# Kernel optimization log

Hardware: AMD Instinct MI355X
Metric: run time of the kernel (lower is better)

The kernel has to match this reference:

```python
import jax, jax.numpy as jnp
import numpy as np

K = 3            # kernel_size
S = 4            # up_factor
VMAX = 1.0
TAU = 0.5
CENTER_BIAS = 2.5
SMOOTH_RES = 0.15
C_IN = 21
HIDDEN = 48
B_, H0, W0 = 4, 81, 81
CTR = K // 2      # = 1, also GL recursion depth M


def _dir_step_diff(k):
    """Precompute (base_pos - base_neg) per direction/step: [8, M+1, k, k]."""
    c = k // 2
    dirs = np.array([[1, 0], [1, 1], [0, 1], [-1, 1], [-1, 0], [-1, -1], [0, -1], [1, -1]], np.float32)
    dirs = dirs / (np.linalg.norm(dirs, axis=1, keepdims=True) + 1e-8)
    yy, xx = np.meshgrid(np.arange(k), np.arange(k), indexing='ij')
    rel = np.stack([yy - c, xx - c], -1).astype(np.float32)
    diff = np.zeros((8, c + 1, k, k), np.float32)
    for d in range(8):
        v = dirs[d]
        proj = rel[..., 0] * v[1] + rel[..., 1] * v[0]
        step = np.clip(np.round(proj), -c, c).astype(np.int64)
        for m in range(c + 1):
            diff[d, m] = (step == m).astype(np.float32) - (step == -m).astype(np.float32)
    return diff

DIFF = jnp.asarray(_dir_step_diff(K))  # [8, M+1, K, K]


def conv3x3(x, w, b):
    y = jax.lax.conv_general_dilated(x, w, (1, 1), 'SAME',
                                     dimension_numbers=('NCHW', 'OIHW', 'NCHW'))
    return y + b[None, :, None, None]


def bilinear_up(x, s):
    """F.interpolate(scale_factor=s, mode='bilinear', align_corners=True)."""
    B, C, h, w = x.shape
    H, W = h * s, w * s
    ys = jnp.linspace(0.0, h - 1.0, H)
    xs = jnp.linspace(0.0, w - 1.0, W)
    y0 = jnp.clip(jnp.floor(ys).astype(jnp.int32), 0, h - 2)
    x0 = jnp.clip(jnp.floor(xs).astype(jnp.int32), 0, w - 2)
    wy = (ys - y0)[:, None]
    wx = (xs - x0)[None, :]
    x00 = x[:, :, y0][:, :, :, x0]
    x01 = x[:, :, y0][:, :, :, x0 + 1]
    x10 = x[:, :, y0 + 1][:, :, :, x0]
    x11 = x[:, :, y0 + 1][:, :, :, x0 + 1]
    return (x00 * (1 - wy) * (1 - wx) + x01 * (1 - wy) * wx
            + x10 * wy * (1 - wx) + x11 * wy * wx)


def setup_inputs() -> dict:
    key = jax.random.key(0)
    ks = jax.random.split(key, 6)
    wn = lambda k, shape: jax.random.normal(k, shape, jnp.float32) * 0.05
    return {
        'x': jax.random.normal(ks[0], (B_, C_IN, H0, W0), jnp.float32),
        'w1o': wn(ks[1], (HIDDEN, C_IN, 3, 3)), 'b1o': jnp.zeros((HIDDEN,), jnp.float32),
        'w2o': wn(ks[2], (8, HIDDEN, 3, 3)), 'b2o': jnp.zeros((8,), jnp.float32),
        'w1g': wn(ks[3], (HIDDEN, C_IN, 3, 3)), 'b1g': jnp.zeros((HIDDEN,), jnp.float32),
        'w2g': wn(ks[4], (1, HIDDEN, 3, 3)), 'b2g': jnp.zeros((1,), jnp.float32),
        'beta': jnp.asarray(1.6, jnp.float32),
    }


def reference(x, w1o, b1o, w2o, b2o, w1g, b1g, w2g, b2g, beta):
    B, C, h, w = x.shape
    c = CTR
    # heads
    raw_v = conv3x3(jax.nn.relu(conv3x3(x, w1o, b1o)), w2o, b2o)          # [B,8,h,w]
    g = jax.nn.sigmoid(conv3x3(jax.nn.relu(conv3x3(x, w1g, b1g)), w2g, b2g))  # [B,1,h,w]
    v = VMAX * jnp.tanh(raw_v)
    # Gruenwald-Letnikov coefficients, M = center (=1 for k=3)
    coeffs = [jnp.ones_like(v)]
    wm = coeffs[0]
    for m in range(1, c + 1):
        wm = wm * (v - m + 1.0) / m * -1.0
        coeffs.append(wm)
    coeff = jnp.stack(coeffs, axis=2)                                      # [B,8,M+1,h,w]
    # direction kernels, averaged over the 8 directions
    ker = jnp.einsum('bdmhw,dmkl->bklhw', coeff, DIFF) / 8.0               # [B,K,K,h,w]
    mask_pre = ker.reshape(B, K * K, h, w)
    ci = c * K + c
    # NOTE: torch adds center_bias in-place on a view of ker -> ker itself is biased too
    mask_pre = mask_pre.at[:, ci].add(CENTER_BIAS)
    ker_b = mask_pre.reshape(B, K, K, h, w)
    mask_lp = jax.nn.softmax(mask_pre / TAU, axis=1)                       # [B,9,h,w]
    # unfold 3x3 window with reflect padding
    xp = jnp.pad(x, ((0, 0), (0, 0), (c, c), (c, c)), mode='reflect')
    patches = jnp.stack([xp[:, :, i:i + h, j:j + w]
                         for i in range(K) for j in range(K)], axis=2)     # [B,C,9,h,w]
    rep2 = lambda a, ax: jnp.repeat(jnp.repeat(a, S, axis=ax), S, axis=ax + 1)
    neigh = rep2(patches, 3)                                               # [B,C,9,H,W]
    mask_lp_u = rep2(mask_lp, 2)                                           # [B,9,H,W]
    g_up = rep2(g, 2)                                                      # [B,1,H,W]
    x_up = bilinear_up(x, S)                                               # [B,C,H,W]
    y_lp_out = jnp.einsum('bcnHW,bnHW->bcHW', neigh, mask_lp_u)
    lam = SMOOTH_RES * (1.0 - g_up)
    y_lp = x_up + lam * (y_lp_out - x_up)
    # highpass branch (mode='both')
    ker_hp = ker_b - ker_b.mean(axis=(1, 2), keepdims=True)
    ker_hp = ker_hp / (jnp.abs(ker_hp).sum(axis=(1, 2), keepdims=True) + 1e-8)
    mask_hp = rep2(ker_hp.reshape(B, K * K, h, w), 2)
    y_hp = jnp.einsum('bcnHW,bnHW->bcHW', neigh, mask_hp)
    y = y_lp + jnp.tanh(beta) * g_up * y_hp
    return (y, v, g_up)
```

## Files before the change

### kernel.cpp

```cpp
#include <hip/hip_runtime.h>
#include <math.h>

#define B_N   4
#define CIN   21
#define HIDC  48
#define H0    81
#define NP    6561
#define HH    324
#define NPH   104976

__device__ __forceinline__ float tanh_fast(float x) {
    float e = __expf(2.f * x);
    return 1.f - 2.f / (e + 1.f);
}

__global__ __launch_bounds__(256) void k1_conv1(
    const float* __restrict__ x,
    const float* __restrict__ w1o, const float* __restrict__ b1o,
    const float* __restrict__ w1g, const float* __restrict__ b1g,
    float* __restrict__ hid_o, float* __restrict__ hid_g)
{
    __shared__ __align__(16) float xs[CIN * 18 * 20];
    __shared__ __align__(16) float wt[189 * 32];
    __shared__ float bs[32];
    const int tid = threadIdx.x;
    const int tile = blockIdx.x, ocg = blockIdx.y, b = blockIdx.z;
    const int ty0 = (tile / 6) * 16, tx0 = (tile % 6) * 16;
    const float* xb = x + (size_t)b * CIN * NP;

    for (int pos = tid; pos < 324; pos += 256) {
        const int yy = pos / 18, xx = pos - yy * 18;
        const int gy = ty0 - 1 + yy, gx = tx0 - 1 + xx;
        const bool ok = ((unsigned)gy < (unsigned)H0) && ((unsigned)gx < (unsigned)H0);
        const int gidx = gy * H0 + gx;
        #pragma unroll 3
        for (int ic = 0; ic < CIN; ic++)
            xs[ic * 360 + yy * 20 + xx] = ok ? xb[ic * NP + gidx] : 0.f;
    }
    for (int i = tid; i < 189 * 32; i += 256) {
        const int ict = i >> 5, oc = i & 31;
        const int oc96 = ocg * 32 + oc;
        wt[i] = (oc96 < 48) ? w1o[oc96 * 189 + ict] : w1g[(oc96 - 48) * 189 + ict];
    }
    if (tid < 32) {
        const int oc96 = ocg * 32 + tid;
        bs[tid] = (oc96 < 48) ? b1o[oc96] : b1g[oc96 - 48];
    }
    __syncthreads();

    const int og = tid >> 6;
    const int q  = tid & 63;
    const int qy = q >> 2, qx4 = (q & 3) * 4;
    const int oc8 = og * 8;

    float acc[4][8];
    #pragma unroll
    for (int i = 0; i < 4; i++)
        #pragma unroll
        for (int j = 0; j < 8; j++) acc[i][j] = bs[oc8 + j];

    for (int ic = 0; ic < CIN; ic++) {
        #pragma unroll
        for (int ky = 0; ky < 3; ky++) {
            const float4 f0 = *(const float4*)&xs[ic * 360 + (qy + ky) * 20 + qx4];
            const float4 f1 = *(const float4*)&xs[ic * 360 + (qy + ky) * 20 + qx4 + 4];
            const float xw[8] = {f0.x, f0.y, f0.z, f0.w, f1.x, f1.y, f1.z, f1.w};
            #pragma unroll
            for (int kx = 0; kx < 3; kx++) {
                const float4 wa = *(const float4*)&wt[(ic * 9 + ky * 3 + kx) * 32 + oc8];
                const float4 wb = *(const float4*)&wt[(ic * 9 + ky * 3 + kx) * 32 + oc8 + 4];
                const float wj[8] = {wa.x, wa.y, wa.z, wa.w, wb.x, wb.y, wb.z, wb.w};
                #pragma unroll
                for (int i = 0; i < 4; i++)
                    #pragma unroll
                    for (int j = 0; j < 8; j++)
                        acc[i][j] = fmaf(xw[i + kx], wj[j], acc[i][j]);
            }
        }
    }

    const int oy = ty0 + qy;
    const int ox0 = tx0 + qx4;
    if (oy < H0) {
        #pragma unroll
        for (int j = 0; j < 8; j++) {
            const int oc96 = ocg * 32 + oc8 + j;
            float* base = (oc96 < 48)
                ? hid_o + ((size_t)b * HIDC + oc96) * NP
                : hid_g + ((size_t)b * HIDC + (oc96 - 48)) * NP;
            if (ox0 + 3 < H0) {
                *reinterpret_cast<float4*>(base + oy * H0 + ox0) =
                    make_float4(fmaxf(acc[0][j], 0.f), fmaxf(acc[1][j], 0.f),
                                fmaxf(acc[2][j], 0.f), fmaxf(acc[3][j], 0.f));
            } else {
                #pragma unroll
                for (int i = 0; i < 4; i++)
                    if (ox0 + i < H0) base[oy * H0 + ox0 + i] = fmaxf(acc[i][j], 0.f);
            }
        }
    }
}

__global__ __launch_bounds__(256) void k2_conv2_masks(
    const float* __restrict__ hid_o, const float* __restrict__ hid_g,
    const float* __restrict__ w2o, const float* __restrict__ b2o,
    const float* __restrict__ w2g, const float* __restrict__ b2g,
    float* __restrict__ v_out,
    float* __restrict__ g_buf, float* __restrict__ m_lp, float* __restrict__ m_hp)
{
    __shared__ __align__(16) float wo_s[HIDC * 9 * 8];
    __shared__ float wg_s[HIDC * 9];
    __shared__ float red[4][32][12];
    __shared__ float res_s[32][28];
    const int tid = threadIdx.x;
    const int b = blockIdx.y;

    for (int i = tid; i < HIDC * 9 * 8; i += 256) {
        const int d = i / (HIDC * 9), r = i - d * (HIDC * 9);
        wo_s[r * 8 + d] = w2o[i];
    }
    for (int i = tid; i < HIDC * 9; i += 256) wg_s[i] = w2g[i];
    __syncthreads();

    const int pxl = tid & 31;
    const int s   = tid >> 5;
    const int w   = tid >> 6;
    const int px  = blockIdx.x * 32 + pxl;
    const bool valid = (px < NP);
    const int oy = px / H0, ox = px - oy * H0;
    const int ic0 = s * 6;
    const float* po = hid_o + ((size_t)b * HIDC + ic0) * NP;
    const float* pg = hid_g + ((size_t)b * HIDC + ic0) * NP;

    float a[8] = {0.f, 0.f, 0.f, 0.f, 0.f, 0.f, 0.f, 0.f};
    float ag = 0.f;

    #pragma unroll 1
    for (int ky = 0; ky < 3; ky++) {
        const int iy = oy + ky - 1;
        const bool rok = valid && ((unsigned)iy < (unsigned)H0);
        #pragma unroll
        for (int kx = 0; kx < 3; kx++) {
            const int ix = ox + kx - 1;
            const bool ok = rok && ((unsigned)ix < (unsigned)H0);
            const int off = iy * H0 + ix;
            const int tap = ky * 3 + kx;
            #pragma unroll
            for (int j = 0; j < 6; j++) {
                const float vo = ok ? po[j * NP + off] : 0.f;
                const float vg = ok ? pg[j * NP + off] : 0.f;
                const int wb = ((ic0 + j) * 9 + tap) * 8;
                const float4 wA = *(const float4*)&wo_s[wb];
                const float4 wB = *(const float4*)&wo_s[wb + 4];
                a[0] = fmaf(vo, wA.x, a[0]); a[1] = fmaf(vo, wA.y, a[1]);
                a[2] = fmaf(vo, wA.z, a[2]); a[3] = fmaf(vo, wA.w, a[3]);
                a[4] = fmaf(vo, wB.x, a[4]); a[5] = fmaf(vo, wB.y, a[5]);
                a[6] = fmaf(vo, wB.z, a[6]); a[7] = fmaf(vo, wB.w, a[7]);
                ag = fmaf(vg, wg_s[(ic0 + j) * 9 + tap], ag);
            }
        }
    }

    #pragma unroll
    for (int n = 0; n < 8; n++) a[n] += __shfl_xor(a[n], 32);
    ag += __shfl_xor(ag, 32);
    if ((tid & 32) == 0) {
        #pragma unroll
        for (int n = 0; n < 8; n++) red[w][pxl][n] = a[n];
        red[w][pxl][8] = ag;
    }
    __syncthreads();

    if (tid < 32 && valid) {
        float v[8];
        #pragma unroll
        for (int n = 0; n < 8; n++)
            v[n] = tanh_fast(red[0][tid][n] + red[1][tid][n] + red[2][tid][n]
                             + red[3][tid][n] + b2o[n]);
        const float agf = red[0][tid][8] + red[1][tid][8] + red[2][tid][8]
                        + red[3][tid][8] + b2g[0];
        const float g = 1.f / (1.f + __expf(-agf));

        constexpr float DT[8][9] = {
            {-1, 0, 1, -1, 0, 1, -1, 0, 1},
            {-1,-1, 0, -1, 0, 1,  0, 1, 1},
            {-1,-1,-1,  0, 0, 0,  1, 1, 1},
            { 0,-1,-1,  1, 0,-1,  1, 1, 0},
            { 1, 0,-1,  1, 0,-1,  1, 0,-1},
            { 1, 1, 0,  1, 0,-1,  0,-1,-1},
            { 1, 1, 1,  0, 0, 0, -1,-1,-1},
            { 0, 1, 1, -1, 0, 1, -1,-1, 0}};
        float ker[9];
        #pragma unroll
        for (int n = 0; n < 9; n++) {
            float t = 0.f;
            #pragma unroll
            for (int d = 0; d < 8; d++) t += v[d] * DT[d][n];
            ker[n] = -0.125f * t;
        }
        ker[4] += 2.5f;
        float mx = ker[0];
        #pragma unroll
        for (int n = 1; n < 9; n++) mx = fmaxf(mx, ker[n]);
        float exn[9], sum = 0.f;
        #pragma unroll
        for (int n = 0; n < 9; n++) { exn[n] = __expf((ker[n] - mx) * 2.0f); sum += exn[n]; }
        const float rs = 1.f / sum;
        float mean = 0.f;
        #pragma unroll
        for (int n = 0; n < 9; n++) mean += ker[n];
        mean *= (1.f / 9.f);
        float den = 1e-8f;
        #pragma unroll
        for (int n = 0; n < 9; n++) den += fabsf(ker[n] - mean);
        const float rd = 1.f / den;

        #pragma unroll
        for (int n = 0; n < 8; n++) res_s[tid][n] = v[n];
        res_s[tid][8] = g;
        #pragma unroll
        for (int n = 0; n < 9; n++) {
            res_s[tid][9 + n]  = exn[n] * rs;
            res_s[tid][18 + n] = (ker[n] - mean) * rd;
        }
    }
    __syncthreads();

    const int px0 = blockIdx.x * 32;
    for (int j = tid; j < 27 * 32; j += 256) {
        const int plane = j >> 5, pl = j & 31;
        const int p = px0 + pl;
        if (p >= NP) continue;
        const float val = res_s[pl][plane];
        float* dst;
        if (plane < 8)        dst = v_out + ((size_t)b * 8 + plane) * NP;
        else if (plane == 8)  dst = g_buf + (size_t)b * NP;
        else if (plane < 18)  dst = m_lp + ((size_t)b * 9 + (plane - 9)) * NP;
        else                  dst = m_hp + ((size_t)b * 9 + (plane - 18)) * NP;
        dst[p] = val;
    }
}

__global__ __launch_bounds__(256) void k4_up(
    const float* __restrict__ x, const float* __restrict__ g_buf,
    const float* __restrict__ m_lp, const float* __restrict__ m_hp,
    const float* __restrict__ beta,
    float* __restrict__ y_out, float* __restrict__ gup_out)
{
    const int tid = threadIdx.x;
    if (tid >= 243) return;
    const int c = blockIdx.y;
    const int b = blockIdx.z;
    const int H = blockIdx.x * 3 + tid / 81;
    const int wq = tid % 81;
    const int h0r = H >> 2;
    const int lpx = h0r * H0 + wq;
    const float g = g_buf[(size_t)b * NP + lpx];
    if (c == CIN) {
        *reinterpret_cast<float4*>(gup_out + (size_t)b * NPH + H * HH + wq * 4) =
            make_float4(g, g, g, g);
        return;
    }
    float ml[9], mh[9];
    const float* mlb = m_lp + (size_t)b * 9 * NP + lpx;
    const float* mhb = m_hp + (size_t)b * 9 * NP + lpx;
    #pragma unroll
    for (int n = 0; n < 9; n++) { ml[n] = mlb[n * NP]; mh[n] = mhb[n * NP]; }
    const float* xc = x + ((size_t)b * CIN + c) * NP;
    float p[3][3];
    #pragma unroll
    for (int ky = 0; ky < 3; ky++) {
        int iy = h0r + ky - 1;
        iy = iy < 0 ? -iy : (iy > H0 - 1 ? 2 * (H0 - 1) - iy : iy);
        #pragma unroll
        for (int kx = 0; kx < 3; kx++) {
            int ix = wq + kx - 1;
            ix = ix < 0 ? -ix : (ix > H0 - 1 ? 2 * (H0 - 1) - ix : ix);
            p[ky][kx] = xc[iy * H0 + ix];
        }
    }
    float alp = 0.f, ahp = 0.f;
    #pragma unroll
    for (int ky = 0; ky < 3; ky++)
        #pragma unroll
        for (int kx = 0; kx < 3; kx++) {
            alp = fmaf(p[ky][kx], ml[ky * 3 + kx], alp);
            ahp = fmaf(p[ky][kx], mh[ky * 3 + kx], ahp);
        }
    const float tb = tanh_fast(beta[0]);
    const float lam = 0.15f * (1.f - g);
    const float gh = tb * g;
    const float ysf = (float)H * (80.f / 323.f);
    int y0 = (int)ysf;
    if (y0 > H0 - 2) y0 = H0 - 2;
    const float wy = ysf - (float)y0;
    const int sy = y0 - h0r + 1;
    float res[4];
    #pragma unroll
    for (int i = 0; i < 4; i++) {
        const int W = wq * 4 + i;
        const float xsf = (float)W * (80.f / 323.f);
        int x0 = (int)xsf;
        if (x0 > H0 - 2) x0 = H0 - 2;
        const float wx = xsf - (float)x0;
        const int sx = x0 - wq + 1;
        const float x00 = sy == 0 ? (sx == 0 ? p[0][0] : p[0][1]) : (sx == 0 ? p[1][0] : p[1][1]);
        const float x01 = sy == 0 ? (sx == 0 ? p[0][1] : p[0][2]) : (sx == 0 ? p[1][1] : p[1][2]);
        const float x10 = sy == 0 ? (sx == 0 ? p[1][0] : p[1][1]) : (sx == 0 ? p[2][0] : p[2][1]);
        const float x11 = sy == 0 ? (sx == 0 ? p[1][1] : p[1][2]) : (sx == 0 ? p[2][1] : p[2][2]);
        const float top = x00 + (x01 - x00) * wx;
        const float bot = x10 + (x11 - x10) * wx;
        const float xup = top + (bot - top) * wy;
        res[i] = xup + lam * (alp - xup) + gh * ahp;
    }
    *reinterpret_cast<float4*>(y_out + ((size_t)b * CIN + c) * NPH + H * HH + wq * 4) =
        make_float4(res[0], res[1], res[2], res[3]);
}

extern "C" void kernel_launch(void* const* d_in, const int* in_sizes, int n_in,
                              void* d_out, int out_size, void* d_ws, size_t ws_size,
                              hipStream_t stream)
{
    const float* x    = (const float*)d_in[0];
    const float* w1o  = (const float*)d_in[1];
    const float* b1o  = (const float*)d_in[2];
    const float* w2o  = (const float*)d_in[3];
    const float* b2o  = (const float*)d_in[4];
    const float* w1g  = (const float*)d_in[5];
    const float* b1g  = (const float*)d_in[6];
    const float* w2g  = (const float*)d_in[7];
    const float* b2g  = (const float*)d_in[8];
    const float* beta = (const float*)d_in[9];
    float* out = (float*)d_out;
    float* wsf = (float*)d_ws;

    float* hid_o = wsf;
    float* hid_g = hid_o + (size_t)B_N * HIDC * NP;
    float* m_lp  = hid_g + (size_t)B_N * HIDC * NP;
    float* m_hp  = m_lp + (size_t)B_N * 9 * NP;
    float* g_buf = m_hp + (size_t)B_N * 9 * NP;

    float* y_out = out;
    float* v_out = out + (size_t)B_N * CIN * NPH;
    float* gup   = v_out + (size_t)B_N * 8 * NP;

    k1_conv1<<<dim3(36, 3, B_N), 256, 0, stream>>>(x, w1o, b1o, w1g, b1g, hid_o, hid_g);
    k2_conv2_masks<<<dim3((NP + 31) / 32, B_N), 256, 0, stream>>>(
        hid_o, hid_g, w2o, b2o, w2g, b2g, v_out, g_buf, m_lp, m_hp);
    k4_up<<<dim3(108, CIN + 1, B_N), 256, 0, stream>>>(x, g_buf, m_lp, m_hp, beta, y_out, gup);
}
```

Before: 153.8 us.

## Restructure conv1 to per-pixel blocks and k4_up to per-row shared staging

conv1 drops the shared-memory input tile. Each thread now computes one pixel for 12 output channels and reads x straight from global memory, with the grid split into 8 channel groups. The upsample kernel now handles one low-res row per block: it stages the masks, g and three reflected x rows for 10-11 channels in shared memory, and computes the low-pass and high-pass weighted sums once per low-res pixel. Those sums are then reused for all 4x4 output pixels. The aim is to remove the redundant mask loads and neighbourhood sums that the old upsample repeated 4 times per output row, at the cost of lower register-level reuse in conv1.

```diff
diff --git a/kernel.cpp b/kernel.cpp
--- a/kernel.cpp
+++ b/kernel.cpp
@@ -20,84 +20,61 @@
     const float* __restrict__ w1g, const float* __restrict__ b1g,
     float* __restrict__ hid_o, float* __restrict__ hid_g)
 {
-    __shared__ __align__(16) float xs[CIN * 18 * 20];
-    __shared__ __align__(16) float wt[189 * 32];
-    __shared__ float bs[32];
+    __shared__ __align__(16) float wt[189 * 12];
+    __shared__ float bs[12];
     const int tid = threadIdx.x;
-    const int tile = blockIdx.x, ocg = blockIdx.y, b = blockIdx.z;
-    const int ty0 = (tile / 6) * 16, tx0 = (tile % 6) * 16;
+    const int grp = blockIdx.y;
+    const int b   = blockIdx.z;
+    const bool head_o = (grp < 4);
+    const int ocb = (grp & 3) * 12;
+    const float* wsrc = head_o ? w1o : w1g;
+    for (int i = tid; i < 189 * 12; i += 256) {
+        const int ict = i / 12, oc = i - ict * 12;
+        wt[i] = wsrc[(ocb + oc) * 189 + ict];
+    }
+    if (tid < 12) bs[tid] = (head_o ? b1o : b1g)[ocb + tid];
+    __syncthreads();
+
+    const int px = blockIdx.x * 256 + tid;
+    const bool valid = (px < NP);
+    const int oy = px / H0, ox = px - oy * H0;
     const float* xb = x + (size_t)b * CIN * NP;
 
-    for (int pos = tid; pos < 324; pos += 256) {
-        const int yy = pos / 18, xx = pos - yy * 18;
-        const int gy = ty0 - 1 + yy, gx = tx0 - 1 + xx;
-        const bool ok = ((unsigned)gy < (unsigned)H0) && ((unsigned)gx < (unsigned)H0);
-        const int gidx = gy * H0 + gx;
-        #pragma unroll 3
-        for (int ic = 0; ic < CIN; ic++)
-            xs[ic * 360 + yy * 20 + xx] = ok ? xb[ic * NP + gidx] : 0.f;
-    }
-    for (int i = tid; i < 189 * 32; i += 256) {
-        const int ict = i >> 5, oc = i & 31;
-        const int oc96 = ocg * 32 + oc;
-        wt[i] = (oc96 < 48) ? w1o[oc96 * 189 + ict] : w1g[(oc96 - 48) * 189 + ict];
-    }
-    if (tid < 32) {
-        const int oc96 = ocg * 32 + tid;
-        bs[tid] = (oc96 < 48) ? b1o[oc96] : b1g[oc96 - 48];
-    }
-    __syncthreads();
-
-    const int og = tid >> 6;
-    const int q  = tid & 63;
-    const int qy = q >> 2, qx4 = (q & 3) * 4;
-    const int oc8 = og * 8;
-
-    float acc[4][8];
+    float acc[12];
     #pragma unroll
-    for (int i = 0; i < 4; i++)
-        #pragma unroll
-        for (int j = 0; j < 8; j++) acc[i][j] = bs[oc8 + j];
+    for (int j = 0; j < 12; j++) acc[j] = bs[j];
 
     for (int ic = 0; ic < CIN; ic++) {
+        const float* xc = xb + ic * NP;
+        float xv[9];
         #pragma unroll
         for (int ky = 0; ky < 3; ky++) {
-            const float4 f0 = *(const float4*)&xs[ic * 360 + (qy + ky) * 20 + qx4];
-            const float4 f1 = *(const float4*)&xs[ic * 360 + (qy + ky) * 20 + qx4 + 4];
-            const float xw[8] = {f0.x, f0.y, f0.z, f0.w, f1.x, f1.y, f1.z, f1.w};
+            const int iy = oy + ky - 1;
+            const bool rok = valid && ((unsigned)iy < (unsigned)H0);
             #pragma unroll
             for (int kx = 0; kx < 3; kx++) {
-                const float4 wa = *(const float4*)&wt[(ic * 9 + ky * 3 + kx) * 32 + oc8];
-                const float4 wb = *(const float4*)&wt[(ic * 9 + ky * 3 + kx) * 32 + oc8 + 4];
-                const float wj[8] = {wa.x, wa.y, wa.z, wa.w, wb.x, wb.y, wb.z, wb.w};
-                #pragma unroll
-                for (int i = 0; i < 4; i++)
-                    #pragma unroll
-                    for (int j = 0; j < 8; j++)
-                        acc[i][j] = fmaf(xw[i + kx], wj[j], acc[i][j]);
+                const int ix = ox + kx - 1;
+                const bool ok = rok && ((unsigned)ix < (unsigned)H0);
+                xv[ky * 3 + kx] = ok ? xc[iy * H0 + ix] : 0.f;
             }
         }
-    }
-
-    const int oy = ty0 + qy;
-    const int ox0 = tx0 + qx4;
-    if (oy < H0) {
-        #pragma unroll
-        for (int j = 0; j < 8; j++) {
-            const int oc96 = ocg * 32 + oc8 + j;
-            float* base = (oc96 < 48)
-                ? hid_o + ((size_t)b * HIDC + oc96) * NP
-                : hid_g + ((size_t)b * HIDC + (oc96 - 48)) * NP;
-            if (ox0 + 3 < H0) {
-                *reinterpret_cast<float4*>(base + oy * H0 + ox0) =
-                    make_float4(fmaxf(acc[0][j], 0.f), fmaxf(acc[1][j], 0.f),
-                                fmaxf(acc[2][j], 0.f), fmaxf(acc[3][j], 0.f));
-            } else {
-                #pragma unroll
-                for (int i = 0; i < 4; i++)
-                    if (ox0 + i < H0) base[oy * H0 + ox0 + i] = fmaxf(acc[i][j], 0.f);
-            }
-        }
+        #pragma unroll
+        for (int tap = 0; tap < 9; tap++) {
+            const float4 w0 = *(const float4*)&wt[(ic * 9 + tap) * 12];
+            const float4 w1 = *(const float4*)&wt[(ic * 9 + tap) * 12 + 4];
+            const float4 w2 = *(const float4*)&wt[(ic * 9 + tap) * 12 + 8];
+            const float wj[12] = {w0.x, w0.y, w0.z, w0.w, w1.x, w1.y, w1.z, w1.w,
+                                  w2.x, w2.y, w2.z, w2.w};
+            const float xvt = xv[tap];
+            #pragma unroll
+            for (int j = 0; j < 12; j++) acc[j] = fmaf(xvt, wj[j], acc[j]);
+        }
+    }
+
+    if (valid) {
+        float* outp = (head_o ? hid_o : hid_g) + ((size_t)b * HIDC + ocb) * NP + px;
+        #pragma unroll
+        for (int j = 0; j < 12; j++) outp[j * NP] = fmaxf(acc[j], 0.f);
     }
 }
 
@@ -247,74 +224,102 @@
     const float* __restrict__ beta,
     float* __restrict__ y_out, float* __restrict__ gup_out)
 {
-    const int tid = threadIdx.x;
-    if (tid >= 243) return;
-    const int c = blockIdx.y;
-    const int b = blockIdx.z;
-    const int H = blockIdx.x * 3 + tid / 81;
-    const int wq = tid % 81;
-    const int h0r = H >> 2;
-    const int lpx = h0r * H0 + wq;
-    const float g = g_buf[(size_t)b * NP + lpx];
-    if (c == CIN) {
-        *reinterpret_cast<float4*>(gup_out + (size_t)b * NPH + H * HH + wq * 4) =
-            make_float4(g, g, g, g);
-        return;
-    }
-    float ml[9], mh[9];
-    const float* mlb = m_lp + (size_t)b * 9 * NP + lpx;
-    const float* mhb = m_hp + (size_t)b * 9 * NP + lpx;
-    #pragma unroll
-    for (int n = 0; n < 9; n++) { ml[n] = mlb[n * NP]; mh[n] = mhb[n * NP]; }
-    const float* xc = x + ((size_t)b * CIN + c) * NP;
-    float p[3][3];
-    #pragma unroll
-    for (int ky = 0; ky < 3; ky++) {
-        int iy = h0r + ky - 1;
-        iy = iy < 0 ? -iy : (iy > H0 - 1 ? 2 * (H0 - 1) - iy : iy);
-        #pragma unroll
-        for (int kx = 0; kx < 3; kx++) {
-            int ix = wq + kx - 1;
-            ix = ix < 0 ? -ix : (ix > H0 - 1 ? 2 * (H0 - 1) - ix : ix);
-            p[ky][kx] = xc[iy * H0 + ix];
-        }
-    }
-    float alp = 0.f, ahp = 0.f;
-    #pragma unroll
-    for (int ky = 0; ky < 3; ky++)
-        #pragma unroll
-        for (int kx = 0; kx < 3; kx++) {
-            alp = fmaf(p[ky][kx], ml[ky * 3 + kx], alp);
-            ahp = fmaf(p[ky][kx], mh[ky * 3 + kx], ahp);
-        }
+    __shared__ float ml_s[9][81];
+    __shared__ float mh_s[9][81];
+    __shared__ float g_s[81];
+    __shared__ float xrow[3][11][84];
+    __shared__ float alp_s[11][84];
+    __shared__ float ahp_s[11][84];
+    const int tid  = threadIdx.x;
+    const int h0r  = blockIdx.x;
+    const int ygrp = blockIdx.y;
+    const int b    = blockIdx.z;
+    const int c0   = ygrp * 11;
+    const int nc   = (ygrp == 0) ? 11 : 10;
+
+    const int rb = h0r * H0;
+    for (int i = tid; i < 19 * 81; i += 256) {
+        const int pl = i / 81, wq = i - pl * 81;
+        if (pl < 9)       ml_s[pl][wq] = m_lp[((size_t)b * 9 + pl) * NP + rb + wq];
+        else if (pl < 18) mh_s[pl - 9][wq] = m_hp[((size_t)b * 9 + (pl - 9)) * NP + rb + wq];
+        else              g_s[wq] = g_buf[(size_t)b * NP + rb + wq];
+    }
+    const int r0 = (h0r == 0) ? 1 : h0r - 1;
+    const int r2 = (h0r == H0 - 1) ? H0 - 2 : h0r + 1;
+    const int rr[3] = {r0, h0r, r2};
+    for (int i = tid; i < 3 * nc * 81; i += 256) {
+        const int t = i / (nc * 81), rem = i - t * nc * 81;
+        const int cc = rem / 81, wq = rem - cc * 81;
+        xrow[t][cc][wq] = x[((size_t)b * CIN + c0 + cc) * NP + rr[t] * H0 + wq];
+    }
+    __syncthreads();
+
+    for (int i = tid; i < nc * 81; i += 256) {
+        const int cc = i / 81, wq = i - cc * 81;
+        const int xm = (wq == 0) ? 1 : wq - 1;
+        const int xp = (wq == H0 - 1) ? H0 - 2 : wq + 1;
+        float alp = 0.f, ahp = 0.f;
+        #pragma unroll
+        for (int t = 0; t < 3; t++) {
+            const float p0 = xrow[t][cc][xm];
+            const float p1 = xrow[t][cc][wq];
+            const float p2 = xrow[t][cc][xp];
+            alp += p0 * ml_s[t * 3 + 0][wq] + p1 * ml_s[t * 3 + 1][wq] + p2 * ml_s[t * 3 + 2][wq];
+            ahp += p0 * mh_s[t * 3 + 0][wq] + p1 * mh_s[t * 3 + 1][wq] + p2 * mh_s[t * 3 + 2][wq];
+        }
+        alp_s[cc][wq] = alp;
+        ahp_s[cc][wq] = ahp;
+    }
+    __syncthreads();
+
     const float tb = tanh_fast(beta[0]);
-    const float lam = 0.15f * (1.f - g);
-    const float gh = tb * g;
-    const float ysf = (float)H * (80.f / 323.f);
-    int y0 = (int)ysf;
-    if (y0 > H0 - 2) y0 = H0 - 2;
-    const float wy = ysf - (float)y0;
-    const int sy = y0 - h0r + 1;
-    float res[4];
-    #pragma unroll
-    for (int i = 0; i < 4; i++) {
-        const int W = wq * 4 + i;
-        const float xsf = (float)W * (80.f / 323.f);
-        int x0 = (int)xsf;
-        if (x0 > H0 - 2) x0 = H0 - 2;
-        const float wx = xsf - (float)x0;
-        const int sx = x0 - wq + 1;
-        const float x00 = sy == 0 ? (sx == 0 ? p[0][0] : p[0][1]) : (sx == 0 ? p[1][0] : p[1][1]);
-        const float x01 = sy == 0 ? (sx == 0 ? p[0][1] : p[0][2]) : (sx == 0 ? p[1][1] : p[1][2]);
-        const float x10 = sy == 0 ? (sx == 0 ? p[1][0] : p[1][1]) : (sx == 0 ? p[2][0] : p[2][1]);
-        const float x11 = sy == 0 ? (sx == 0 ? p[1][1] : p[1][2]) : (sx == 0 ? p[2][1] : p[2][2]);
-        const float top = x00 + (x01 - x00) * wx;
-        const float bot = x10 + (x11 - x10) * wx;
-        const float xup = top + (bot - top) * wy;
-        res[i] = xup + lam * (alp - xup) + gh * ahp;
-    }
-    *reinterpret_cast<float4*>(y_out + ((size_t)b * CIN + c) * NPH + H * HH + wq * 4) =
-        make_float4(res[0], res[1], res[2], res[3]);
+    for (int i = tid; i < 11 * 4 * 81; i += 256) {
+        const int pl = i / 324, rem = i - pl * 324;
+        const int dh = rem / 81, wq = rem - dh * 81;
+        const int H = h0r * 4 + dh;
+        if (ygrp == 1 && pl == 10) {
+            const float g = g_s[wq];
+            *reinterpret_cast<float4*>(gup_out + (size_t)b * NPH + H * HH + wq * 4) =
+                make_float4(g, g, g, g);
+            continue;
+        }
+        const int cc = pl;
+        const int c = c0 + pl;
+        const float g = g_s[wq];
+        const float lam = 0.15f * (1.f - g);
+        const float gh = tb * g;
+        const float alp = alp_s[cc][wq];
+        const float ahp = ahp_s[cc][wq];
+        const float ysf = (float)H * (80.f / 323.f);
+        int y0 = (int)ysf;
+        if (y0 > H0 - 2) y0 = H0 - 2;
+        const float wy = ysf - (float)y0;
+        const int sy = y0 - h0r + 1;
+        const int xm = (wq == 0) ? 1 : wq - 1;
+        const int xp = (wq == H0 - 1) ? H0 - 2 : wq + 1;
+        const float a0 = xrow[sy][cc][(wq == 0) ? 0 : xm];
+        const float a1 = xrow[sy][cc][wq];
+        const float a2 = xrow[sy][cc][(wq == H0 - 1) ? H0 - 1 : xp];
+        const float b0 = xrow[sy + 1][cc][(wq == 0) ? 0 : xm];
+        const float b1 = xrow[sy + 1][cc][wq];
+        const float b2 = xrow[sy + 1][cc][(wq == H0 - 1) ? H0 - 1 : xp];
+        float res[4];
+        #pragma unroll
+        for (int k = 0; k < 4; k++) {
+            const int W = wq * 4 + k;
+            const float xsf = (float)W * (80.f / 323.f);
+            int x0 = (int)xsf;
+            if (x0 > H0 - 2) x0 = H0 - 2;
+            const float wx = xsf - (float)x0;
+            const int sx = x0 - wq + 1;
+            const float top = (sx == 0) ? a0 + (a1 - a0) * wx : a1 + (a2 - a1) * wx;
+            const float bot = (sx == 0) ? b0 + (b1 - b0) * wx : b1 + (b2 - b1) * wx;
+            const float xup = top + (bot - top) * wy;
+            res[k] = xup + lam * (alp - xup) + gh * ahp;
+        }
+        *reinterpret_cast<float4*>(y_out + ((size_t)b * CIN + c) * NPH + H * HH + wq * 4) =
+            make_float4(res[0], res[1], res[2], res[3]);
+    }
 }
 
 extern "C" void kernel_launch(void* const* d_in, const int* in_sizes, int n_in,
@@ -344,8 +349,9 @@
     float* v_out = out + (size_t)B_N * CIN * NPH;
     float* gup   = v_out + (size_t)B_N * 8 * NP;
 
-    k1_conv1<<<dim3(36, 3, B_N), 256, 0, stream>>>(x, w1o, b1o, w1g, b1g, hid_o, hid_g);
+    k1_conv1<<<dim3((NP + 255) / 256, 8, B_N), 256, 0, stream>>>(
+        x, w1o, b1o, w1g, b1g, hid_o, hid_g);
     k2_conv2_masks<<<dim3((NP + 31) / 32, B_N), 256, 0, stream>>>(
         hid_o, hid_g, w2o, b2o, w2g, b2g, v_out, g_buf, m_lp, m_hp);
-    k4_up<<<dim3(108, CIN + 1, B_N), 256, 0, stream>>>(x, g_buf, m_lp, m_hp, beta, y_out, gup);
-}
+    k4_up<<<dim3(H0, 2, B_N), 256, 0, stream>>>(x, g_buf, m_lp, m_hp, beta, y_out, gup);
+}
```

After: 153.3 us. Within noise of the previous version (-0.3%).
